# Optimization experiments

Measured on AMD Instinct MI355X. Metric: run time of the kernel, lower is better.

## Reference

```python
import jax, jax.numpy as jnp
import numpy as np

T, B, E, H = 512, 64, 256, 256


def setup_inputs() -> dict:
    key = jax.random.key(0)
    ks = jax.random.split(key, 14)
    def p(k, shape, s=0.05):
        return jax.random.normal(k, shape, dtype=jnp.float32) * s
    return {
        "inputs": jax.random.normal(ks[0], (T, B, E), dtype=jnp.float32),
        # attention params (nn.Parameter torch.randn -> unit scale)
        "rot": jax.random.normal(ks[1], (E, E), dtype=jnp.float32),
        "ent": jax.random.normal(ks[2], (E, E), dtype=jnp.float32),
        # gate linears: stored as (in, out) so y = x @ W + b (same math as torch Linear)
        "Wf": p(ks[3], (E + H, H)), "bf": jnp.zeros((H,), jnp.float32),
        "Wi": p(ks[4], (E + H, H)), "bi": jnp.zeros((H,), jnp.float32),
        "Wu": p(ks[5], (E + H, H)), "bu": jnp.zeros((H,), jnp.float32),
        "Wo": p(ks[6], (E + H, H)), "bo": jnp.zeros((H,), jnp.float32),
        "Wc": p(ks[7], (E, H)),     "bc": jnp.zeros((H,), jnp.float32),
    }


def reference(inputs, rot, ent, Wf, bf, Wi, bi, Wu, bu, Wo, bo, Wc, bc):
    t, b, e = inputs.shape
    h = Wf.shape[1]
    # --- one-shot self-attention (ClassicalSelfAttention) ---
    inp = inputs.transpose(1, 0, 2)                       # [B,T,E]
    q = jnp.einsum('bte,ef->btf', inp, rot)
    k = jnp.einsum('bte,ef->btf', inp, ent)
    scores = jax.nn.softmax(jnp.einsum('btf,bsf->bts', q, k) / jnp.sqrt(jnp.float32(e)), axis=-1)
    context = jnp.einsum('bts,bse->bte', scores, inp).transpose(1, 0, 2)  # [T,B,E]
    # context projection is time-invariant -> precompute as one big GEMM
    ctx_proj = context @ Wc + bc                          # [T,B,H]
    # --- recurrent LSTM cell over time via scan ---
    def step(carry, xs):
        hx, cx = carry
        x, cp = xs
        combined = jnp.concatenate([x, hx + cp], axis=1)  # [B,E+H]
        f = jax.nn.sigmoid(combined @ Wf + bf)
        i = jax.nn.sigmoid(combined @ Wi + bi)
        g = jnp.tanh(combined @ Wu + bu)
        o = jax.nn.sigmoid(combined @ Wo + bo)
        cx = f * cx + i * g
        hx = o * jnp.tanh(cx)
        return (hx, cx), hx
    hx0 = jnp.zeros((b, h), inputs.dtype)
    cx0 = jnp.zeros((b, h), inputs.dtype)
    (hx, cx), outputs = jax.lax.scan(step, (hx0, cx0), (inputs, ctx_proj))
    return outputs, hx, cx
```

## Files before the change

### kernel.cpp

```cpp
#include <hip/hip_runtime.h>

#define T_ 512
#define B_ 64
#define E_ 256
#define H_ 256

typedef __attribute__((ext_vector_type(8))) short short8_t;
typedef __attribute__((ext_vector_type(4))) float floatx4;

__device__ __forceinline__ unsigned short f2bf(float f) {
  unsigned int u = __float_as_uint(f);
  u += 0x7FFFu + ((u >> 16) & 1u);
  return (unsigned short)(u >> 16);
}
__device__ __forceinline__ float bf2f(unsigned short s) {
  return __uint_as_float(((unsigned int)s) << 16);
}
__device__ __forceinline__ float fast_tanh(float x) {
  float e = __expf(-2.0f * x);
  return 2.0f / (1.0f + e) - 1.0f;
}

__global__ __launch_bounds__(256) void qk_kernel(
    const float* __restrict__ inp, const float* __restrict__ rot,
    const float* __restrict__ ent, float* __restrict__ qo, float* __restrict__ ko)
{
  __shared__ __align__(16) float As[16][136];
  __shared__ __align__(16) float B1[16][68];
  __shared__ __align__(16) float B2[16][68];
  const int tid = threadIdx.x;
  const int m0 = blockIdx.y * 128, n0 = blockIdx.x * 64;
  const int lk = tid & 15, lm = tid >> 4;
  const int ln = tid & 63, lkb = tid >> 6;
  const int tx = tid & 15, ty = tid >> 4;
  float acc1[8][4], acc2[8][4];
#pragma unroll
  for (int i = 0; i < 8; ++i)
#pragma unroll
    for (int j = 0; j < 4; ++j) { acc1[i][j] = 0.f; acc2[i][j] = 0.f; }

  for (int k0 = 0; k0 < 256; k0 += 16) {
    __syncthreads();
#pragma unroll
    for (int p = 0; p < 8; ++p) {
      int m = lm + p * 16;
      As[lk][m] = inp[(size_t)(m0 + m) * 256 + k0 + lk];
    }
#pragma unroll
    for (int p = 0; p < 4; ++p) {
      int kk = lkb + p * 4;
      B1[kk][ln] = rot[(size_t)(k0 + kk) * 256 + n0 + ln];
      B2[kk][ln] = ent[(size_t)(k0 + kk) * 256 + n0 + ln];
    }
    __syncthreads();
#pragma unroll
    for (int kk = 0; kk < 16; ++kk) {
      floatx4 a_lo = *(const floatx4*)&As[kk][ty * 8];
      floatx4 a_hi = *(const floatx4*)&As[kk][ty * 8 + 4];
      floatx4 b1v = *(const floatx4*)&B1[kk][tx * 4];
      floatx4 b2v = *(const floatx4*)&B2[kk][tx * 4];
#pragma unroll
      for (int i = 0; i < 4; ++i) {
        float alo = a_lo[i], ahi = a_hi[i];
#pragma unroll
        for (int j = 0; j < 4; ++j) {
          acc1[i][j]     += alo * b1v[j];
          acc1[i + 4][j] += ahi * b1v[j];
          acc2[i][j]     += alo * b2v[j];
          acc2[i + 4][j] += ahi * b2v[j];
        }
      }
    }
  }
#pragma unroll
  for (int i = 0; i < 8; ++i) {
    size_t row = (size_t)(m0 + ty * 8 + i);
    float4 v1 = make_float4(acc1[i][0], acc1[i][1], acc1[i][2], acc1[i][3]);
    float4 v2 = make_float4(acc2[i][0], acc2[i][1], acc2[i][2], acc2[i][3]);
    *(float4*)&qo[row * 256 + n0 + tx * 4] = v1;
    *(float4*)&ko[row * 256 + n0 + tx * 4] = v2;
  }
}

__global__ __launch_bounds__(256) void scores_kernel(
    const float* __restrict__ q, const float* __restrict__ k, float* __restrict__ S)
{
  __shared__ __align__(16) float As[16][136];
  __shared__ __align__(16) float Bs[16][68];
  const int tid = threadIdx.x;
  const int b = blockIdx.z;
  const int m0 = blockIdx.y * 128, n0 = blockIdx.x * 64;
  const int lk = tid & 15, lm = tid >> 4;
  const int tx = tid & 15, ty = tid >> 4;
  float acc[8][4];
#pragma unroll
  for (int i = 0; i < 8; ++i)
#pragma unroll
    for (int j = 0; j < 4; ++j) acc[i][j] = 0.f;

  const float* Ab = q + (size_t)b * 256;
  const float* Bb = k + (size_t)b * 256;
  for (int k0 = 0; k0 < 256; k0 += 16) {
    __syncthreads();
#pragma unroll
    for (int p = 0; p < 8; ++p) {
      int m = lm + p * 16;
      As[lk][m] = Ab[(size_t)(m0 + m) * 16384 + k0 + lk];
    }
#pragma unroll
    for (int p = 0; p < 4; ++p) {
      int n = lm + p * 16;
      Bs[lk][n] = Bb[(size_t)(n0 + n) * 16384 + k0 + lk];
    }
    __syncthreads();
#pragma unroll
    for (int kk = 0; kk < 16; ++kk) {
      floatx4 a_lo = *(const floatx4*)&As[kk][ty * 8];
      floatx4 a_hi = *(const floatx4*)&As[kk][ty * 8 + 4];
      floatx4 bv = *(const floatx4*)&Bs[kk][tx * 4];
#pragma unroll
      for (int i = 0; i < 4; ++i) {
        float alo = a_lo[i], ahi = a_hi[i];
#pragma unroll
        for (int j = 0; j < 4; ++j) {
          acc[i][j]     += alo * bv[j];
          acc[i + 4][j] += ahi * bv[j];
        }
      }
    }
  }
#pragma unroll
  for (int i = 0; i < 8; ++i) {
    size_t off = (size_t)b * 262144 + (size_t)(m0 + ty * 8 + i) * 512 + n0 + tx * 4;
    float4 v = make_float4(acc[i][0] * 0.0625f, acc[i][1] * 0.0625f,
                           acc[i][2] * 0.0625f, acc[i][3] * 0.0625f);
    *(float4*)&S[off] = v;
  }
}

__global__ __launch_bounds__(256) void softmax_kernel(float* __restrict__ S)
{
  float* p = S + (size_t)blockIdx.x * 512;
  const int tid = threadIdx.x;
  float x0 = p[tid], x1 = p[tid + 256];
  float m = fmaxf(x0, x1);
#pragma unroll
  for (int off = 32; off > 0; off >>= 1) m = fmaxf(m, __shfl_xor(m, off));
  __shared__ float red[8];
  const int wv = tid >> 6;
  if ((tid & 63) == 0) red[wv] = m;
  __syncthreads();
  m = fmaxf(fmaxf(red[0], red[1]), fmaxf(red[2], red[3]));
  float e0 = __expf(x0 - m);
  float e1 = __expf(x1 - m);
  float s = e0 + e1;
#pragma unroll
  for (int off = 32; off > 0; off >>= 1) s += __shfl_xor(s, off);
  if ((tid & 63) == 0) red[4 + wv] = s;
  __syncthreads();
  s = red[4] + red[5] + red[6] + red[7];
  float r = 1.0f / s;
  p[tid] = e0 * r;
  p[tid + 256] = e1 * r;
}

__global__ __launch_bounds__(256) void context_kernel(
    const float* __restrict__ P, const float* __restrict__ inp, float* __restrict__ ctx)
{
  __shared__ __align__(16) float As[16][136];
  __shared__ __align__(16) float Bs[16][68];
  const int tid = threadIdx.x;
  const int b = blockIdx.z;
  const int m0 = blockIdx.y * 128, e0 = blockIdx.x * 64;
  const int lk = tid & 15, lm = tid >> 4;
  const int ln = tid & 63, lkb = tid >> 6;
  const int tx = tid & 15, ty = tid >> 4;
  float acc[8][4];
#pragma unroll
  for (int i = 0; i < 8; ++i)
#pragma unroll
    for (int j = 0; j < 4; ++j) acc[i][j] = 0.f;

  const float* Ab = P + (size_t)b * 262144;
  for (int k0 = 0; k0 < 512; k0 += 16) {
    __syncthreads();
#pragma unroll
    for (int p = 0; p < 8; ++p) {
      int m = lm + p * 16;
      As[lk][m] = Ab[(size_t)(m0 + m) * 512 + k0 + lk];
    }
#pragma unroll
    for (int p = 0; p < 4; ++p) {
      int kk = lkb + p * 4;
      Bs[kk][ln] = inp[(size_t)(k0 + kk) * 16384 + b * 256 + e0 + ln];
    }
    __syncthreads();
#pragma unroll
    for (int kk = 0; kk < 16; ++kk) {
      floatx4 a_lo = *(const floatx4*)&As[kk][ty * 8];
      floatx4 a_hi = *(const floatx4*)&As[kk][ty * 8 + 4];
      floatx4 bv = *(const floatx4*)&Bs[kk][tx * 4];
#pragma unroll
      for (int i = 0; i < 4; ++i) {
        float alo = a_lo[i], ahi = a_hi[i];
#pragma unroll
        for (int j = 0; j < 4; ++j) {
          acc[i][j]     += alo * bv[j];
          acc[i + 4][j] += ahi * bv[j];
        }
      }
    }
  }
#pragma unroll
  for (int i = 0; i < 8; ++i) {
    size_t off = (size_t)(m0 + ty * 8 + i) * 16384 + (size_t)b * 256 + e0 + tx * 4;
    float4 v = make_float4(acc[i][0], acc[i][1], acc[i][2], acc[i][3]);
    *(float4*)&ctx[off] = v;
  }
}

__global__ __launch_bounds__(256) void cp_kernel(
    const float* __restrict__ ctx, const float* __restrict__ Wc,
    const float* __restrict__ bc, float* __restrict__ cp)
{
  __shared__ __align__(16) float As[16][136];
  __shared__ __align__(16) float Bs[16][68];
  const int tid = threadIdx.x;
  const int m0 = blockIdx.y * 128, n0 = blockIdx.x * 64;
  const int lk = tid & 15, lm = tid >> 4;
  const int ln = tid & 63, lkb = tid >> 6;
  const int tx = tid & 15, ty = tid >> 4;
  float acc[8][4];
#pragma unroll
  for (int i = 0; i < 8; ++i)
#pragma unroll
    for (int j = 0; j < 4; ++j) acc[i][j] = 0.f;

  for (int k0 = 0; k0 < 256; k0 += 16) {
    __syncthreads();
#pragma unroll
    for (int p = 0; p < 8; ++p) {
      int m = lm + p * 16;
      As[lk][m] = ctx[(size_t)(m0 + m) * 256 + k0 + lk];
    }
#pragma unroll
    for (int p = 0; p < 4; ++p) {
      int kk = lkb + p * 4;
      Bs[kk][ln] = Wc[(size_t)(k0 + kk) * 256 + n0 + ln];
    }
    __syncthreads();
#pragma unroll
    for (int kk = 0; kk < 16; ++kk) {
      floatx4 a_lo = *(const floatx4*)&As[kk][ty * 8];
      floatx4 a_hi = *(const floatx4*)&As[kk][ty * 8 + 4];
      floatx4 bv = *(const floatx4*)&Bs[kk][tx * 4];
#pragma unroll
      for (int i = 0; i < 4; ++i) {
        float alo = a_lo[i], ahi = a_hi[i];
#pragma unroll
        for (int j = 0; j < 4; ++j) {
          acc[i][j]     += alo * bv[j];
          acc[i + 4][j] += ahi * bv[j];
        }
      }
    }
  }
  float b0 = bc[n0 + tx * 4 + 0], b1 = bc[n0 + tx * 4 + 1];
  float b2 = bc[n0 + tx * 4 + 2], b3 = bc[n0 + tx * 4 + 3];
#pragma unroll
  for (int i = 0; i < 8; ++i) {
    size_t row = (size_t)(m0 + ty * 8 + i);
    float4 v = make_float4(acc[i][0] + b0, acc[i][1] + b1, acc[i][2] + b2, acc[i][3] + b3);
    *(float4*)&cp[row * 256 + n0 + tx * 4] = v;
  }
}

__global__ __launch_bounds__(256) void pack_w(
    const float* __restrict__ Wf, const float* __restrict__ Wi,
    const float* __restrict__ Wu, const float* __restrict__ Wo,
    const float* __restrict__ bfv, const float* __restrict__ biv,
    const float* __restrict__ buv, const float* __restrict__ bov,
    unsigned short* __restrict__ Wt, float* __restrict__ bcat)
{
  const int n = blockIdx.x;
  const int g = n >> 8, h = n & 255;
  const float* W = (g == 0) ? Wf : (g == 1) ? Wi : (g == 2) ? Wu : Wo;
  const float* bb = (g == 0) ? bfv : (g == 1) ? biv : (g == 2) ? buv : bov;
  for (int k = threadIdx.x; k < 512; k += 256)
    Wt[(size_t)n * 512 + k] = f2bf(W[(size_t)k * 256 + h]);
  if (threadIdx.x == 0) bcat[n] = bb[h];
}

__global__ __launch_bounds__(256) void gemm_pre(
    const float* __restrict__ x, const float* __restrict__ cp,
    const unsigned short* __restrict__ Wt, const float* __restrict__ bcat,
    unsigned short* __restrict__ pre)
{
  __shared__ __align__(16) unsigned short As[64 * 40];
  __shared__ __align__(16) unsigned short Bs[64 * 40];
  const int tid = threadIdx.x;
  const int n0 = blockIdx.x * 64, m0 = blockIdx.y * 64;
  const int lane = tid & 63, wv = tid >> 6;
  const int lm = lane & 15, qd = lane >> 4;
  const int sr = tid >> 2, sk = (tid & 3) * 8;
  floatx4 acc[4] = {{0.f,0.f,0.f,0.f},{0.f,0.f,0.f,0.f},
                    {0.f,0.f,0.f,0.f},{0.f,0.f,0.f,0.f}};
  for (int k0 = 0; k0 < 512; k0 += 32) {
    const float* Asrc = (k0 < 256)
        ? (x  + (size_t)(m0 + sr) * 256 + k0 + sk)
        : (cp + (size_t)(m0 + sr) * 256 + (k0 - 256) + sk);
    float4 a0 = *(const float4*)Asrc;
    float4 a1 = *(const float4*)(Asrc + 4);
    short8_t av;
    av[0] = (short)f2bf(a0.x); av[1] = (short)f2bf(a0.y);
    av[2] = (short)f2bf(a0.z); av[3] = (short)f2bf(a0.w);
    av[4] = (short)f2bf(a1.x); av[5] = (short)f2bf(a1.y);
    av[6] = (short)f2bf(a1.z); av[7] = (short)f2bf(a1.w);
    short8_t bv = *(const short8_t*)&Wt[(size_t)(n0 + sr) * 512 + k0 + sk];
    *(short8_t*)&As[sr * 40 + sk] = av;
    *(short8_t*)&Bs[sr * 40 + sk] = bv;
    __syncthreads();
    short8_t af = *(const short8_t*)&As[(wv * 16 + lm) * 40 + qd * 8];
#pragma unroll
    for (int nt = 0; nt < 4; ++nt) {
      short8_t bf = *(const short8_t*)&Bs[(nt * 16 + lm) * 40 + qd * 8];
      acc[nt] = __builtin_amdgcn_mfma_f32_16x16x32_bf16(af, bf, acc[nt], 0, 0, 0);
    }
    __syncthreads();
  }
#pragma unroll
  for (int nt = 0; nt < 4; ++nt) {
    int col = n0 + nt * 16 + lm;
    float bb = bcat[col];
    int col2 = ((col & 255) << 2) | (col >> 8);
#pragma unroll
    for (int r = 0; r < 4; ++r) {
      int row = m0 + wv * 16 + qd * 4 + r;
      pre[(size_t)row * 1024 + col2] = f2bf(acc[nt][r] + bb);
    }
  }
}

__global__ __launch_bounds__(256, 1) void scan_kernel(
    const unsigned short* __restrict__ pre,
    const unsigned short* __restrict__ Wt,
    float* __restrict__ out, unsigned long long* __restrict__ hxT)
{
  __shared__ __align__(16) unsigned short hl[2][16 * 264];
  const int tid = threadIdx.x;
  const int bg = blockIdx.x >> 2;
  const int cg = blockIdx.x & 3;
  const int lane = tid & 63;
  const int w = tid >> 6;
  const int qd = lane >> 4;
  const int lh = lane & 15;

  {
    unsigned long long* z = (unsigned long long*)hl;
    for (int i = tid; i < 2112; i += 256) z[i] = 0ull;
  }

  short8_t wreg[4][8];
#pragma unroll
  for (int g = 0; g < 4; ++g)
#pragma unroll
    for (int kc = 0; kc < 8; ++kc)
      wreg[g][kc] = *(const short8_t*)&Wt[(size_t)(g * 256 + cg * 64 + w * 16 + lh) * 512
                                          + 256 + kc * 32 + qd * 8];

  const unsigned long long* pq = (const unsigned long long*)pre;
  const int orow0 = bg * 16 + qd * 4;
  const int hcol = cg * 64 + w * 16 + lh;
  unsigned long long pcur[4], pnext[4];
#pragma unroll
  for (int r = 0; r < 4; ++r)
    pcur[r] = pq[(size_t)(orow0 + r) * 256 + hcol];

  float cst[4] = {0.f, 0.f, 0.f, 0.f};
  const int cg1 = (cg + 1) & 3, cg2 = (cg + 2) & 3, cg3 = (cg + 3) & 3;
  const int prow = tid >> 4, pcolq = tid & 15;

  __syncthreads();

#pragma unroll 1
  for (int t = 0; t < 512; ++t) {
    unsigned long long* hlqR = (unsigned long long*)hl[t & 1];
    unsigned long long* hlqW = (unsigned long long*)hl[(t + 1) & 1];

    if (t > 0) {
      const unsigned long long* sbase = hxT + (size_t)((t - 1) * 4 + bg) * 1024;
      const unsigned long long* s0 = sbase + (size_t)cg1 * 256;
      const unsigned long long* s1 = sbase + (size_t)cg2 * 256;
      const unsigned long long* s2 = sbase + (size_t)cg3 * 256;
      unsigned long long d0, d1, d2;
      bool ok;
      do {
        d0 = __hip_atomic_load(&s0[tid], __ATOMIC_RELAXED, __HIP_MEMORY_SCOPE_AGENT);
        d1 = __hip_atomic_load(&s1[tid], __ATOMIC_RELAXED, __HIP_MEMORY_SCOPE_AGENT);
        d2 = __hip_atomic_load(&s2[tid], __ATOMIC_RELAXED, __HIP_MEMORY_SCOPE_AGENT);
        ok = ((unsigned int)d0 != 0xFFFFFFFFu) && ((unsigned int)(d0 >> 32) != 0xFFFFFFFFu)
          && ((unsigned int)d1 != 0xFFFFFFFFu) && ((unsigned int)(d1 >> 32) != 0xFFFFFFFFu)
          && ((unsigned int)d2 != 0xFFFFFFFFu) && ((unsigned int)(d2 >> 32) != 0xFFFFFFFFu);
      } while (!__all((int)ok));
      hlqR[prow * 66 + cg1 * 16 + pcolq] = d0;
      hlqR[prow * 66 + cg2 * 16 + pcolq] = d1;
      hlqR[prow * 66 + cg3 * 16 + pcolq] = d2;
    }

    if (t < 511) {
      size_t base = (size_t)((t + 1) * 64 + orow0) * 256 + hcol;
#pragma unroll
      for (int r = 0; r < 4; ++r)
        pnext[r] = pq[base + (size_t)r * 256];
    }

    __syncthreads();

    const unsigned short* hb = hl[t & 1];
    floatx4 acc[4] = {{0.f,0.f,0.f,0.f},{0.f,0.f,0.f,0.f},
                      {0.f,0.f,0.f,0.f},{0.f,0.f,0.f,0.f}};
#pragma unroll
    for (int kc = 0; kc < 8; ++kc) {
      short8_t av = *(const short8_t*)&hb[lh * 264 + kc * 32 + qd * 8];
#pragma unroll
      for (int g = 0; g < 4; ++g)
        acc[g] = __builtin_amdgcn_mfma_f32_16x16x32_bf16(av, wreg[g][kc], acc[g], 0, 0, 0);
    }

    float h[4];
#pragma unroll
    for (int r = 0; r < 4; ++r) {
      unsigned long long pv = pcur[r];
      float xf = acc[0][r] + bf2f((unsigned short)pv);
      float xi = acc[1][r] + bf2f((unsigned short)(pv >> 16));
      float xu = acc[2][r] + bf2f((unsigned short)(pv >> 32));
      float xo = acc[3][r] + bf2f((unsigned short)(pv >> 48));
      float fg = 1.0f / (1.0f + __expf(-xf));
      float ig = 1.0f / (1.0f + __expf(-xi));
      float gg = fast_tanh(xu);
      float og = 1.0f / (1.0f + __expf(-xo));
      float cc = fg * cst[r] + ig * gg;
      cst[r] = cc;
      h[r] = og * fast_tanh(cc);
    }

    float t0c, t1c, t2c, t3c;
    {
      float e0 = __shfl_xor(h[0], 1);
      float e1 = __shfl_xor(h[1], 1);
      float e2 = __shfl_xor(h[2], 1);
      float e3 = __shfl_xor(h[3], 1);
      bool odd = (lane & 1);
      float b0 = odd ? e1 : h[0];
      float b1 = odd ? h[1] : e0;
      float b2 = odd ? e3 : h[2];
      float b3 = odd ? h[3] : e2;
      float f0 = __shfl_xor(b0, 2);
      float f1 = __shfl_xor(b1, 2);
      float f2 = __shfl_xor(b2, 2);
      float f3 = __shfl_xor(b3, 2);
      bool hi = (lane & 2);
      t0c = hi ? f2 : b0;
      t1c = hi ? f3 : b1;
      t2c = hi ? b2 : f0;
      t3c = hi ? b3 : f1;
    }
    unsigned long long hp = (unsigned long long)f2bf(t0c)
        | ((unsigned long long)f2bf(t1c) << 16)
        | ((unsigned long long)f2bf(t2c) << 32)
        | ((unsigned long long)f2bf(t3c) << 48);
    const int orow = qd * 4 + (lane & 3);
    const int ocolq = w * 4 + (lh >> 2);

    __hip_atomic_store(&hxT[(size_t)((t * 4 + bg) * 4 + cg) * 256 + orow * 16 + ocolq],
                       hp, __ATOMIC_RELAXED, __HIP_MEMORY_SCOPE_AGENT);
    hlqW[orow * 66 + cg * 16 + ocolq] = hp;
    *(float4*)&out[(size_t)t * 16384 + (size_t)(bg * 16 + orow) * 256 + cg * 64 + ocolq * 4]
        = make_float4(t0c, t1c, t2c, t3c);

    if (t == 511) {
      const size_t hoff = (size_t)512 * 16384;
#pragma unroll
      for (int r = 0; r < 4; ++r) {
        out[hoff + (size_t)(orow0 + r) * 256 + hcol] = h[r];
        out[hoff + 16384 + (size_t)(orow0 + r) * 256 + hcol] = cst[r];
      }
    }
#pragma unroll
    for (int r = 0; r < 4; ++r) pcur[r] = pnext[r];
  }
}

extern "C" void kernel_launch(void* const* d_in, const int* in_sizes, int n_in,
                              void* d_out, int out_size, void* d_ws, size_t ws_size,
                              hipStream_t stream)
{
  const float* inputs = (const float*)d_in[0];
  const float* rot = (const float*)d_in[1];
  const float* ent = (const float*)d_in[2];
  const float* Wf = (const float*)d_in[3];
  const float* bf_ = (const float*)d_in[4];
  const float* Wi = (const float*)d_in[5];
  const float* bi_ = (const float*)d_in[6];
  const float* Wu = (const float*)d_in[7];
  const float* bu_ = (const float*)d_in[8];
  const float* Wo = (const float*)d_in[9];
  const float* bo_ = (const float*)d_in[10];
  const float* Wc = (const float*)d_in[11];
  const float* bc_ = (const float*)d_in[12];
  float* out = (float*)d_out;

  char* ws = (char*)d_ws;
  float* q  = (float*)(ws);
  float* kb = (float*)(ws + (size_t)32 * 1024 * 1024);
  float* S  = (float*)(ws + (size_t)64 * 1024 * 1024);
  unsigned short* pre = (unsigned short*)S;
  float* ctx = q;
  float* cp  = kb;
  unsigned short* Wcat = (unsigned short*)ws;
  float* bcat = (float*)(ws + (size_t)1048576);
  unsigned long long* hxT =
      (unsigned long long*)(ws + (size_t)2 * 1024 * 1024);

  qk_kernel<<<dim3(4, 256), 256, 0, stream>>>(inputs, rot, ent, q, kb);
  scores_kernel<<<dim3(8, 4, 64), 256, 0, stream>>>(q, kb, S);
  softmax_kernel<<<dim3(32768), 256, 0, stream>>>(S);
  context_kernel<<<dim3(4, 4, 64), 256, 0, stream>>>(S, inputs, ctx);
  cp_kernel<<<dim3(4, 256), 256, 0, stream>>>(ctx, Wc, bc_, cp);
  hipMemsetAsync(hxT, 0xFF, (size_t)16 * 1024 * 1024, stream);
  pack_w<<<dim3(1024), 256, 0, stream>>>(Wf, Wi, Wu, Wo, bf_, bi_, bu_, bo_,
                                         Wcat, bcat);
  gemm_pre<<<dim3(16, 512), 256, 0, stream>>>(inputs, cp, Wcat, bcat, pre);
  scan_kernel<<<dim3(16), 256, 0, stream>>>(pre, Wcat, out, hxT);
}
```

Before: 1.756 ms.

## Use split-bf16 MFMA for attention scores and context GEMMs

Replaces the FP32 SIMT tiled GEMMs in the scores and context kernels with bf16 MFMA 16x16x32 instructions. Each operand is split into high and low bf16 parts, and three passes (hi*hi, hi*lo, lo*hi) approximate FP32 accuracy. Tiles become 64x64 with a doubled grid. The change targets the FP32 FMA throughput cost of these batched GEMMs. In exchange it adds conversion work, a transposed scalar LDS store for the context B operand, and slightly lower precision than full FP32.

Result: slower. 1.829 ms (+4.1%).

```diff
diff --git a/kernel.cpp b/kernel.cpp
--- a/kernel.cpp
+++ b/kernel.cpp
@@ -85,56 +85,54 @@
 __global__ __launch_bounds__(256) void scores_kernel(
     const float* __restrict__ q, const float* __restrict__ k, float* __restrict__ S)
 {
-  __shared__ __align__(16) float As[16][136];
-  __shared__ __align__(16) float Bs[16][68];
+  __shared__ __align__(16) unsigned short As[64 * 40];
+  __shared__ __align__(16) unsigned short Bs[64 * 40];
   const int tid = threadIdx.x;
   const int b = blockIdx.z;
-  const int m0 = blockIdx.y * 128, n0 = blockIdx.x * 64;
-  const int lk = tid & 15, lm = tid >> 4;
-  const int tx = tid & 15, ty = tid >> 4;
-  float acc[8][4];
-#pragma unroll
-  for (int i = 0; i < 8; ++i)
-#pragma unroll
-    for (int j = 0; j < 4; ++j) acc[i][j] = 0.f;
-
-  const float* Ab = q + (size_t)b * 256;
-  const float* Bb = k + (size_t)b * 256;
-  for (int k0 = 0; k0 < 256; k0 += 16) {
-    __syncthreads();
-#pragma unroll
-    for (int p = 0; p < 8; ++p) {
-      int m = lm + p * 16;
-      As[lk][m] = Ab[(size_t)(m0 + m) * 16384 + k0 + lk];
-    }
-#pragma unroll
-    for (int p = 0; p < 4; ++p) {
-      int n = lm + p * 16;
-      Bs[lk][n] = Bb[(size_t)(n0 + n) * 16384 + k0 + lk];
-    }
-    __syncthreads();
-#pragma unroll
-    for (int kk = 0; kk < 16; ++kk) {
-      floatx4 a_lo = *(const floatx4*)&As[kk][ty * 8];
-      floatx4 a_hi = *(const floatx4*)&As[kk][ty * 8 + 4];
-      floatx4 bv = *(const floatx4*)&Bs[kk][tx * 4];
-#pragma unroll
-      for (int i = 0; i < 4; ++i) {
-        float alo = a_lo[i], ahi = a_hi[i];
-#pragma unroll
-        for (int j = 0; j < 4; ++j) {
-          acc[i][j]     += alo * bv[j];
-          acc[i + 4][j] += ahi * bv[j];
-        }
-      }
-    }
-  }
-#pragma unroll
-  for (int i = 0; i < 8; ++i) {
-    size_t off = (size_t)b * 262144 + (size_t)(m0 + ty * 8 + i) * 512 + n0 + tx * 4;
-    float4 v = make_float4(acc[i][0] * 0.0625f, acc[i][1] * 0.0625f,
-                           acc[i][2] * 0.0625f, acc[i][3] * 0.0625f);
-    *(float4*)&S[off] = v;
+  const int n0 = blockIdx.x * 64, m0 = blockIdx.y * 64;
+  const int lane = tid & 63, wv = tid >> 6;
+  const int lm = lane & 15, qd = lane >> 4;
+  const int sr = tid >> 2, sk = (tid & 3) * 8;
+  floatx4 acc[4] = {{0.f,0.f,0.f,0.f},{0.f,0.f,0.f,0.f},
+                    {0.f,0.f,0.f,0.f},{0.f,0.f,0.f,0.f}};
+  for (int c = 0; c < 24; ++c) {
+    const int k0 = c * 32;
+    const int off = (k0 & 255) + sk;
+    const bool aLo = (c >= 16);
+    const bool bLo = (c >= 8) && (c < 16);
+    const float* Ap = q + ((size_t)(m0 + sr) * 64 + b) * 256 + off;
+    const float* Bp = k + ((size_t)(n0 + sr) * 64 + b) * 256 + off;
+    float4 a0 = *(const float4*)Ap;  float4 a1 = *(const float4*)(Ap + 4);
+    float4 b0 = *(const float4*)Bp;  float4 b1 = *(const float4*)(Bp + 4);
+    float af_[8] = {a0.x,a0.y,a0.z,a0.w,a1.x,a1.y,a1.z,a1.w};
+    float bf_[8] = {b0.x,b0.y,b0.z,b0.w,b1.x,b1.y,b1.z,b1.w};
+    short8_t av, bv;
+#pragma unroll
+    for (int i = 0; i < 8; ++i) {
+      unsigned short ha = f2bf(af_[i]);
+      av[i] = aLo ? (short)f2bf(af_[i] - bf2f(ha)) : (short)ha;
+      unsigned short hb = f2bf(bf_[i]);
+      bv[i] = bLo ? (short)f2bf(bf_[i] - bf2f(hb)) : (short)hb;
+    }
+    *(short8_t*)&As[sr * 40 + sk] = av;
+    *(short8_t*)&Bs[sr * 40 + sk] = bv;
+    __syncthreads();
+    short8_t af = *(const short8_t*)&As[(wv * 16 + lm) * 40 + qd * 8];
+#pragma unroll
+    for (int nt = 0; nt < 4; ++nt) {
+      short8_t bf = *(const short8_t*)&Bs[(nt * 16 + lm) * 40 + qd * 8];
+      acc[nt] = __builtin_amdgcn_mfma_f32_16x16x32_bf16(af, bf, acc[nt], 0, 0, 0);
+    }
+    __syncthreads();
+  }
+#pragma unroll
+  for (int nt = 0; nt < 4; ++nt) {
+    const int col = n0 + nt * 16 + lm;
+#pragma unroll
+    for (int r = 0; r < 4; ++r) {
+      const int row = m0 + wv * 16 + qd * 4 + r;
+      S[(size_t)b * 262144 + (size_t)row * 512 + col] = acc[nt][r] * 0.0625f;
+    }
   }
 }
 
@@ -167,55 +165,61 @@
 __global__ __launch_bounds__(256) void context_kernel(
     const float* __restrict__ P, const float* __restrict__ inp, float* __restrict__ ctx)
 {
-  __shared__ __align__(16) float As[16][136];
-  __shared__ __align__(16) float Bs[16][68];
+  __shared__ __align__(16) unsigned short As[64 * 40];
+  __shared__ __align__(16) unsigned short Bs[64 * 40];
   const int tid = threadIdx.x;
   const int b = blockIdx.z;
-  const int m0 = blockIdx.y * 128, e0 = blockIdx.x * 64;
-  const int lk = tid & 15, lm = tid >> 4;
-  const int ln = tid & 63, lkb = tid >> 6;
-  const int tx = tid & 15, ty = tid >> 4;
-  float acc[8][4];
-#pragma unroll
-  for (int i = 0; i < 8; ++i)
-#pragma unroll
-    for (int j = 0; j < 4; ++j) acc[i][j] = 0.f;
-
-  const float* Ab = P + (size_t)b * 262144;
-  for (int k0 = 0; k0 < 512; k0 += 16) {
-    __syncthreads();
-#pragma unroll
-    for (int p = 0; p < 8; ++p) {
-      int m = lm + p * 16;
-      As[lk][m] = Ab[(size_t)(m0 + m) * 512 + k0 + lk];
-    }
-#pragma unroll
-    for (int p = 0; p < 4; ++p) {
-      int kk = lkb + p * 4;
-      Bs[kk][ln] = inp[(size_t)(k0 + kk) * 16384 + b * 256 + e0 + ln];
-    }
-    __syncthreads();
-#pragma unroll
-    for (int kk = 0; kk < 16; ++kk) {
-      floatx4 a_lo = *(const floatx4*)&As[kk][ty * 8];
-      floatx4 a_hi = *(const floatx4*)&As[kk][ty * 8 + 4];
-      floatx4 bv = *(const floatx4*)&Bs[kk][tx * 4];
-#pragma unroll
-      for (int i = 0; i < 4; ++i) {
-        float alo = a_lo[i], ahi = a_hi[i];
-#pragma unroll
-        for (int j = 0; j < 4; ++j) {
-          acc[i][j]     += alo * bv[j];
-          acc[i + 4][j] += ahi * bv[j];
-        }
-      }
-    }
-  }
-#pragma unroll
-  for (int i = 0; i < 8; ++i) {
-    size_t off = (size_t)(m0 + ty * 8 + i) * 16384 + (size_t)b * 256 + e0 + tx * 4;
-    float4 v = make_float4(acc[i][0], acc[i][1], acc[i][2], acc[i][3]);
-    *(float4*)&ctx[off] = v;
+  const int e0 = blockIdx.x * 64, m0 = blockIdx.y * 64;
+  const int lane = tid & 63, wv = tid >> 6;
+  const int lm = lane & 15, qd = lane >> 4;
+  const int sr = tid >> 2, sk = (tid & 3) * 8;
+  const int bkk = tid >> 3, be8 = (tid & 7) * 8;
+  floatx4 acc[4] = {{0.f,0.f,0.f,0.f},{0.f,0.f,0.f,0.f},
+                    {0.f,0.f,0.f,0.f},{0.f,0.f,0.f,0.f}};
+  for (int c = 0; c < 48; ++c) {
+    const int k0 = c * 32;
+    const int soff = k0 & 511;
+    const bool aLo = (c >= 32);
+    const bool bLo = (c >= 16) && (c < 32);
+    const float* Ap = P + (size_t)b * 262144 + (size_t)(m0 + sr) * 512 + soff + sk;
+    float4 a0 = *(const float4*)Ap;  float4 a1 = *(const float4*)(Ap + 4);
+    float af_[8] = {a0.x,a0.y,a0.z,a0.w,a1.x,a1.y,a1.z,a1.w};
+    short8_t av;
+#pragma unroll
+    for (int i = 0; i < 8; ++i) {
+      unsigned short ha = f2bf(af_[i]);
+      av[i] = aLo ? (short)f2bf(af_[i] - bf2f(ha)) : (short)ha;
+    }
+    const float* Bp = inp + (size_t)(soff + bkk) * 16384 + (size_t)b * 256 + e0 + be8;
+    float4 b0 = *(const float4*)Bp;  float4 b1 = *(const float4*)(Bp + 4);
+    float bf_[8] = {b0.x,b0.y,b0.z,b0.w,b1.x,b1.y,b1.z,b1.w};
+    unsigned short bq[8];
+#pragma unroll
+    for (int i = 0; i < 8; ++i) {
+      unsigned short hb = f2bf(bf_[i]);
+      bq[i] = bLo ? f2bf(bf_[i] - bf2f(hb)) : hb;
+    }
+    *(short8_t*)&As[sr * 40 + sk] = av;
+#pragma unroll
+    for (int i = 0; i < 8; ++i)
+      Bs[(be8 + i) * 40 + bkk] = bq[i];
+    __syncthreads();
+    short8_t af = *(const short8_t*)&As[(wv * 16 + lm) * 40 + qd * 8];
+#pragma unroll
+    for (int nt = 0; nt < 4; ++nt) {
+      short8_t bf = *(const short8_t*)&Bs[(nt * 16 + lm) * 40 + qd * 8];
+      acc[nt] = __builtin_amdgcn_mfma_f32_16x16x32_bf16(af, bf, acc[nt], 0, 0, 0);
+    }
+    __syncthreads();
+  }
+#pragma unroll
+  for (int nt = 0; nt < 4; ++nt) {
+    const int col = e0 + nt * 16 + lm;
+#pragma unroll
+    for (int r = 0; r < 4; ++r) {
+      const int row = m0 + wv * 16 + qd * 4 + r;
+      ctx[(size_t)row * 16384 + (size_t)b * 256 + col] = acc[nt][r];
+    }
   }
 }
 
@@ -523,9 +527,9 @@
       (unsigned long long*)(ws + (size_t)2 * 1024 * 1024);
 
   qk_kernel<<<dim3(4, 256), 256, 0, stream>>>(inputs, rot, ent, q, kb);
-  scores_kernel<<<dim3(8, 4, 64), 256, 0, stream>>>(q, kb, S);
+  scores_kernel<<<dim3(8, 8, 64), 256, 0, stream>>>(q, kb, S);
   softmax_kernel<<<dim3(32768), 256, 0, stream>>>(S);
-  context_kernel<<<dim3(4, 4, 64), 256, 0, stream>>>(S, inputs, ctx);
+  context_kernel<<<dim3(4, 8, 64), 256, 0, stream>>>(S, inputs, ctx);
   cp_kernel<<<dim3(4, 256), 256, 0, stream>>>(ctx, Wc, bc_, cp);
   hipMemsetAsync(hxT, 0xFF, (size_t)16 * 1024 * 1024, stream);
   pack_w<<<dim3(1024), 256, 0, stream>>>(Wf, Wi, Wu, Wo, bf_, bi_, bu_, bo_,
```
